# Kernel optimization log

Measured on AMD Instinct MI355X. Metric: run time of the kernel, lower is better.

The kernel has to match this reference:

```python
import jax, jax.numpy as jnp
import numpy as np
from jax import lax

V_VOX, T_PTS, D, H, W = 12000, 35, 10, 200, 176
EPS = 1e-5


def _bn(x, g, b, axes, shape):
    m = x.mean(axes, keepdims=True)
    v = x.var(axes, keepdims=True)  # biased var, matches torch BN training stats
    return g.reshape(shape) * (x - m) * lax.rsqrt(v + EPS) + b.reshape(shape)


def _conv3d(x, w, b):
    y = lax.conv_general_dilated(x, w, (1, 1, 1), 'SAME',
                                 dimension_numbers=('NCDHW', 'OIDHW', 'NCDHW'))
    return y + b[None, :, None, None, None]


def _conv2d(x, w, b):
    y = lax.conv_general_dilated(x, w, (1, 1), 'SAME',
                                 dimension_numbers=('NCHW', 'OIHW', 'NCHW'))
    return y + b[None, :, None, None]


def setup_inputs() -> dict:
    key = jax.random.key(0)
    ks = jax.random.split(key, 12)
    voxels = jax.random.normal(ks[0], (1, V_VOX, T_PTS, 4), jnp.float32)
    # unique voxel coordinates (the torch loop overwrites on duplicates; unique avoids ambiguity)
    rng = np.random.default_rng(0)
    flat = rng.choice(D * H * W, size=V_VOX, replace=False)
    z = flat // (H * W); rem = flat % (H * W)
    coords = jnp.asarray(np.stack([z, rem // W, rem % W], axis=1), dtype=jnp.int32)
    s = 0.05
    p = dict(
        w_lin=jax.random.normal(ks[1], (32, 4), jnp.float32) * s,
        b_lin=jnp.zeros((32,), jnp.float32),
        g_bn0=jnp.ones((32,), jnp.float32), be_bn0=jnp.zeros((32,), jnp.float32),
        w_c3a=jax.random.normal(ks[2], (64, 32, 3, 3, 3), jnp.float32) * s,
        b_c3a=jnp.zeros((64,), jnp.float32),
        g_bn1=jnp.ones((64,), jnp.float32), be_bn1=jnp.zeros((64,), jnp.float32),
        w_c3b=jax.random.normal(ks[3], (64, 64, 3, 3, 3), jnp.float32) * s,
        b_c3b=jnp.zeros((64,), jnp.float32),
        g_bn2=jnp.ones((64,), jnp.float32), be_bn2=jnp.zeros((64,), jnp.float32),
        w_r1=jax.random.normal(ks[4], (128, 64, 3, 3), jnp.float32) * s,
        b_r1=jnp.zeros((128,), jnp.float32),
        w_r2=jax.random.normal(ks[5], (8, 128, 1, 1), jnp.float32) * s,
        b_r2=jnp.zeros((8,), jnp.float32),
    )
    return dict(voxels=voxels, coords=coords, **p)


def reference(voxels, coords, w_lin, b_lin, g_bn0, be_bn0,
              w_c3a, b_c3a, g_bn1, be_bn1, w_c3b, b_c3b, g_bn2, be_bn2,
              w_r1, b_r1, w_r2, b_r2):
    B, V, T, C = voxels.shape
    # SimpleVFE: linear -> BN1d (batch stats) -> relu -> max over points
    h = voxels.reshape(B * V * T, C) @ w_lin.T + b_lin          # [BVT,32]
    h = jax.nn.relu(_bn(h, g_bn0, be_bn0, 0, (1, 32)))
    feats = h.reshape(B, V, T, 32).max(axis=2)                  # [B,V,32]
    # fused scatter into dense volume (replaces per-voxel python loop)
    volume = jnp.zeros((B, 32, D, H, W), voxels.dtype)
    volume = volume.at[0, :, coords[:, 0], coords[:, 1], coords[:, 2]].set(feats[0])
    # 3D backbone
    x = jax.nn.relu(_bn(_conv3d(volume, w_c3a, b_c3a), g_bn1, be_bn1, (0, 2, 3, 4), (1, 64, 1, 1, 1)))
    x = jax.nn.relu(_bn(_conv3d(x, w_c3b, b_c3b), g_bn2, be_bn2, (0, 2, 3, 4), (1, 64, 1, 1, 1)))
    x = x.mean(axis=2)                                          # collapse depth -> [B,64,H,W]
    # RPN head
    out = _conv2d(jax.nn.relu(_conv2d(x, w_r1, b_r1)), w_r2, b_r2)  # [B,8,H,W]
    box = jnp.concatenate([out[:, 0:3], jnp.exp(out[:, 3:6]),
                           jnp.tanh(out[:, 6:7]), jax.nn.sigmoid(out[:, 7:8])], axis=1)
    return box
```

## Files before the change

kernel.cpp:

```cpp
#include <hip/hip_runtime.h>
#include <math.h>

#define V_VOX 12000
#define T_PTS 35
#define DD 10
#define HH 200
#define WW 176
#define EPSV 1e-5f

#define DP 12
#define HP 202
#define WP 178
#define PPLN (HP * WP)
#define PVOX (DP * PPLN)
#define NPIX (DD * HH * WW)
#define HWPIX (HH * WW)

typedef _Float16 half_t;
typedef _Float16 f16x8 __attribute__((ext_vector_type(8)));
typedef float f32x16 __attribute__((ext_vector_type(16)));

#define WPA_OFF 0
#define WPB_OFF 110592
#define WPR1_OFF 331776
#define STATS_OFF 479232
#define FEATS_OFF 483328
#define VOLP_OFF 2019328
#define X1P_OFF 29633536
#define Y_OFF 84861952
#define PLANE_OFF 129917952
#define R1OUT_OFF 134520320

#define S_BN0S 0
#define S_BN0Q 32
#define S_BN1S 64
#define S_BN1Q 128
#define S_BN2S 192
#define S_BN2Q 256
#define C0A 320
#define C0B 352
#define C1A 384
#define C1B 448
#define C2A 512
#define C2B 576

__device__ __forceinline__ void gload16(const half_t* g, half_t* l) {
    __builtin_amdgcn_global_load_lds(
        (const __attribute__((address_space(1))) void*)g,
        (__attribute__((address_space(3))) void*)l, 16, 0, 0);
}

__global__ void k_pack(const float* __restrict__ w, half_t* __restrict__ wp,
                       int IC, int NT, int OC) {
    int id = blockIdx.x * 256 + threadIdx.x;
    int OCT = OC >> 5, KH = IC >> 5;
    int total = NT * KH * 2 * OCT * 512;
    if (id >= total) return;
    int j = id & 7;
    int lane = (id >> 3) & 63;
    int rest = id >> 9;
    int ot = rest % OCT; rest /= OCT;
    int khf = rest & 1; rest >>= 1;
    int kh = rest % KH;
    int tap = rest / KH;
    int oc = ot * 32 + (lane & 31);
    int ic = kh * 32 + khf * 16 + (lane >> 5) * 8 + j;
    wp[id] = (half_t)w[(oc * IC + ic) * NT + tap];
}

__global__ void k_vfe_stats(const float4* __restrict__ vox, const float* __restrict__ w_lin,
                            const float* __restrict__ b_lin, float* __restrict__ S) {
    int tid = blockIdx.x * 256 + threadIdx.x;
    int c = threadIdx.x & 31;
    float4 w = ((const float4*)w_lin)[c];
    float bl = b_lin[c];
    float s = 0.f, q = 0.f;
    const int np = V_VOX * T_PTS;
    int stride = gridDim.x * 8;
    for (int p = tid >> 5; p < np; p += stride) {
        float4 v = vox[p];
        float d = v.x * w.x + v.y * w.y + v.z * w.z + v.w * w.w + bl;
        s += d;
        q += d * d;
    }
    s += __shfl_xor(s, 32);
    q += __shfl_xor(q, 32);
    if ((threadIdx.x & 63) < 32) {
        atomicAdd(&S[S_BN0S + c], s);
        atomicAdd(&S[S_BN0Q + c], q);
    }
}

__global__ void k_bn_final(const float* __restrict__ ss, const float* __restrict__ sq,
                           const float* __restrict__ g, const float* __restrict__ be,
                           float* __restrict__ ca, float* __restrict__ cb, int C, float invN) {
    int c = threadIdx.x;
    if (c >= C) return;
    float m = ss[c] * invN;
    float v = sq[c] * invN - m * m;
    float a = g[c] * rsqrtf(v + EPSV);
    ca[c] = a;
    cb[c] = be[c] - m * a;
}

__global__ void k_vfe_max(const float4* __restrict__ vox, const float* __restrict__ w_lin,
                          const float* __restrict__ b_lin, const float* __restrict__ ca,
                          const float* __restrict__ cb, float* __restrict__ feats) {
    int id = blockIdx.x * 256 + threadIdx.x;
    if (id >= V_VOX * 32) return;
    int c = id & 31;
    int v = id >> 5;
    float4 w = ((const float4*)w_lin)[c];
    float bl = b_lin[c], A = ca[c], B = cb[c];
    float m = 0.f;
    for (int t = 0; t < T_PTS; t++) {
        float4 p = vox[v * T_PTS + t];
        float d = p.x * w.x + p.y * w.y + p.z * w.z + p.w * w.w + bl;
        m = fmaxf(m, A * d + B);
    }
    feats[id] = m;
}

__global__ void k_scatter(const float* __restrict__ feats, const int* __restrict__ coords,
                          half_t* __restrict__ volp) {
    int id = blockIdx.x * 256 + threadIdx.x;
    if (id >= V_VOX * 32) return;
    int c = id & 31;
    int v = id >> 5;
    int z = coords[v * 3 + 0];
    int y = coords[v * 3 + 1];
    int x = coords[v * 3 + 2];
    volp[(((z + 1) * HP + (y + 1)) * WP + (x + 1)) * 32 + c] = (half_t)feats[id];
}

template <int KH, int DZ, int OCALL, bool RELU, bool STATS>
__global__ __launch_bounds__(512, 4) void k_conv(const half_t* __restrict__ in,
                                                 size_t khstride,
                                                 const half_t* __restrict__ wp,
                                                 const float* __restrict__ bias,
                                                 half_t* __restrict__ out,
                                                 float* __restrict__ ssum,
                                                 float* __restrict__ ssq) {
    constexpr int OCT = OCALL / 32;
    constexpr int NS = DZ * KH;
    __shared__ __align__(16) half_t tA[1296 * 8];
    __shared__ __align__(16) half_t tB[36 * 512];

    const int tid = threadIdx.x;
    const int lane = tid & 63;
    const int wv = tid >> 6;
    const int yg = wv >> 1;
    const int og = wv & 1;
    const int x0 = blockIdx.x * 16;
    const int y0b = blockIdx.y * 16;
    const int bz = blockIdx.z;
    const int z0 = (DZ == 3) ? bz : 0;
    const int ocb = (DZ == 3) ? 0 : bz * 2;
    const bool valid = (y0b + yg * 4 < HH);
    const int xl = lane & 15;
    const int yrl = (lane >> 4) & 1;
    const int kg = (lane >> 5) & 1;

    int gofsA[3]; bool okA[3];
#pragma unroll
    for (int r = 0; r < 3; ++r) {
        int c = tid + r * 512;
        okA[r] = (c < 1296);
        int cc = okA[r] ? c : 0;
        int p0 = ((cc >> 2) ^ (cc >> 4)) & 1;
        int p = ((cc >> 3) << 1) | p0;
        int q = (cc & 3) ^ (p & 3);
        int row = p / 18, px = p - row * 18;
        int grow = y0b + row;
        if (grow > HP - 1) grow = HP - 1;
        gofsA[r] = (grow * WP + x0 + px) * 32 + q * 8;
    }

    f32x16 acc[2];
#pragma unroll
    for (int m = 0; m < 2; ++m) acc[m] = (f32x16)(0.f);

    auto STAGE = [&](int s) {
        const int dz = s / KH, kh = s % KH;
        const half_t* sl = in + (size_t)kh * khstride
                           + (size_t)(z0 + dz) * (DZ == 3 ? (size_t)PPLN * 32 : 0);
#pragma unroll
        for (int r = 0; r < 3; ++r)
            if (okA[r]) gload16(sl + gofsA[r], &tA[(size_t)(tid + r * 512) * 8]);
#pragma unroll
        for (int r = 0; r < 5; ++r) {
            int c = tid + r * 512;
            if (c < 2304) {
                int u = c >> 6;
                int tl = u >> 2, khf = (u >> 1) & 1, ot = u & 1;
                const half_t* g = wp + ((((size_t)(dz * 9 + tl) * KH + kh) * 2 + khf) * OCT
                                        + ocb + ot) * 512 + lane * 8;
                gload16(g, &tB[(size_t)u * 512 + lane * 8]);
            }
        }
    };

#pragma unroll 1
    for (int s = 0; s < NS; ++s) {
        STAGE(s);
        asm volatile("s_waitcnt vmcnt(0)" ::: "memory");
        __syncthreads();

        if (valid) {
#pragma unroll
            for (int khalf = 0; khalf < 2; ++khalf) {
#pragma unroll
                for (int dx = 0; dx < 3; ++dx) {
#pragma unroll
                    for (int dy = 0; dy < 3; ++dy) {
                        int u = ((dy * 3 + dx) * 2 + khalf) * 2 + og;
                        f16x8 Bf = *(const f16x8*)&tB[u * 512 + lane * 8];
#pragma unroll
                        for (int m = 0; m < 2; ++m) {
                            int p = (yg * 4 + dy + 2 * m + yrl) * 18 + dx + xl;
                            int ph = ((p << 6) | ((khalf * 2 + kg) << 4)) ^ ((p & 7) << 4);
                            f16x8 Af = *(const f16x8*)((const char*)tA + ph);
                            acc[m] = __builtin_amdgcn_mfma_f32_32x32x16_f16(
                                Af, Bf, acc[m], 0, 0, 0);
                        }
                    }
                }
            }
        }
        __syncthreads();
    }

    if (!valid) return;
    float sreg = 0.f, qreg = 0.f;
    int oc = (ocb + og) * 32 + (lane & 31);
    float bv = bias[oc];
#pragma unroll
    for (int m = 0; m < 2; ++m) {
#pragma unroll
        for (int reg = 0; reg < 16; ++reg) {
            int rp = (reg & 3) + 8 * (reg >> 2) + 4 * kg;
            int xx = x0 + (rp & 15);
            int yy = y0b + yg * 4 + 2 * m + (rp >> 4);
            float v = acc[m][reg] + bv;
            if (STATS) { sreg += v; qreg += v * v; }
            float w = RELU ? fmaxf(v, 0.f) : v;
            out[((size_t)(z0 * HH + yy) * WW + xx) * OCALL + oc] = (half_t)w;
        }
    }
    if (STATS) {
        sreg += __shfl_xor(sreg, 32);
        qreg += __shfl_xor(qreg, 32);
        if (lane < 32) {
            atomicAdd(&ssum[oc], sreg);
            atomicAdd(&ssq[oc], qreg);
        }
    }
}

__global__ void k_activate(const half_t* __restrict__ y1, const float* __restrict__ ca,
                           const float* __restrict__ cb, half_t* __restrict__ xp) {
    int id = blockIdx.x * 256 + threadIdx.x;
    if (id >= PVOX * 8) return;
    int c0 = (id & 7) * 8;
    int pix = id >> 3;
    int zp = pix / PPLN;
    int rem = pix - zp * PPLN;
    int yp = rem / WP;
    int xq = rem - yp * WP;
    f16x8 o;
    if (zp >= 1 && zp <= DD && yp >= 1 && yp <= HH && xq >= 1 && xq <= WW) {
        size_t p = ((size_t)((zp - 1) * HH + (yp - 1)) * WW + (xq - 1));
        f16x8 v = *(const f16x8*)(y1 + p * 64 + c0);
#pragma unroll
        for (int j = 0; j < 8; j++)
            o[j] = (half_t)fmaxf(ca[c0 + j] * (float)v[j] + cb[c0 + j], 0.f);
    } else {
#pragma unroll
        for (int j = 0; j < 8; j++) o[j] = (half_t)0.f;
    }
    int khp = c0 >> 5;
    *(f16x8*)(xp + (size_t)khp * PVOX * 32 + (size_t)pix * 32 + (c0 & 31)) = o;
}

__global__ void k_depthmean(const half_t* __restrict__ y2, const float* __restrict__ ca,
                            const float* __restrict__ cb, half_t* __restrict__ plane) {
    int id = blockIdx.x * 256 + threadIdx.x;
    int c = id & 63;
    int pix = id >> 6;
    int yp = pix / WP;
    int xq = pix - yp * WP;
    float val = 0.f;
    if (yp >= 1 && yp <= HH && xq >= 1 && xq <= WW) {
        float A = ca[c], B = cb[c], s = 0.f;
        const half_t* base = y2 + ((size_t)(yp - 1) * WW + (xq - 1)) * 64 + c;
#pragma unroll
        for (int z = 0; z < DD; z++)
            s += fmaxf(A * (float)base[(size_t)z * HWPIX * 64] + B, 0.f);
        val = s * 0.1f;
    }
    int khp = c >> 5;
    plane[(size_t)khp * PPLN * 32 + (size_t)pix * 32 + (c & 31)] = (half_t)val;
}

__global__ void k_r2(const half_t* __restrict__ r1o, const float* __restrict__ w,
                     const float* __restrict__ bias, float* __restrict__ outp) {
    __shared__ float wsm[1024];
    for (int i = threadIdx.x; i < 1024; i += 256) wsm[i] = w[i];
    __syncthreads();
    int p = blockIdx.x * 256 + threadIdx.x;
    if (p >= HWPIX) return;
    float acc[8];
#pragma unroll
    for (int o = 0; o < 8; o++) acc[o] = bias[o];
    const half_t* rb = r1o + (size_t)p * 128;
#pragma unroll 4
    for (int icb = 0; icb < 128; icb += 8) {
        f16x8 v = *(const f16x8*)(rb + icb);
#pragma unroll
        for (int j = 0; j < 8; j++) {
            float vv = (float)v[j];
#pragma unroll
            for (int o = 0; o < 8; o++) acc[o] += vv * wsm[o * 128 + icb + j];
        }
    }
    outp[0 * HWPIX + p] = acc[0];
    outp[1 * HWPIX + p] = acc[1];
    outp[2 * HWPIX + p] = acc[2];
    outp[3 * HWPIX + p] = expf(acc[3]);
    outp[4 * HWPIX + p] = expf(acc[4]);
    outp[5 * HWPIX + p] = expf(acc[5]);
    outp[6 * HWPIX + p] = tanhf(acc[6]);
    outp[7 * HWPIX + p] = 1.f / (1.f + expf(-acc[7]));
}

extern "C" void kernel_launch(void* const* d_in, const int* in_sizes, int n_in,
                              void* d_out, int out_size, void* d_ws, size_t ws_size,
                              hipStream_t stream) {
    const float4* voxels = (const float4*)d_in[0];
    const int* coords = (const int*)d_in[1];
    const float* w_lin = (const float*)d_in[2];
    const float* b_lin = (const float*)d_in[3];
    const float* g_bn0 = (const float*)d_in[4];
    const float* be_bn0 = (const float*)d_in[5];
    const float* w_c3a = (const float*)d_in[6];
    const float* b_c3a = (const float*)d_in[7];
    const float* g_bn1 = (const float*)d_in[8];
    const float* be_bn1 = (const float*)d_in[9];
    const float* w_c3b = (const float*)d_in[10];
    const float* b_c3b = (const float*)d_in[11];
    const float* g_bn2 = (const float*)d_in[12];
    const float* be_bn2 = (const float*)d_in[13];
    const float* w_r1 = (const float*)d_in[14];
    const float* b_r1 = (const float*)d_in[15];
    const float* w_r2 = (const float*)d_in[16];
    const float* b_r2 = (const float*)d_in[17];

    char* ws = (char*)d_ws;
    half_t* wpA = (half_t*)(ws + WPA_OFF);
    half_t* wpB = (half_t*)(ws + WPB_OFF);
    half_t* wpR1 = (half_t*)(ws + WPR1_OFF);
    float* S = (float*)(ws + STATS_OFF);
    float* feats = (float*)(ws + FEATS_OFF);
    half_t* volp = (half_t*)(ws + VOLP_OFF);
    half_t* x1p = (half_t*)(ws + X1P_OFF);
    half_t* Y = (half_t*)(ws + Y_OFF);
    half_t* plane = (half_t*)(ws + PLANE_OFF);
    half_t* r1out = (half_t*)(ws + R1OUT_OFF);
    float* outp = (float*)d_out;

    hipMemsetAsync(S, 0, 320 * sizeof(float), stream);
    hipMemsetAsync(volp, 0, (size_t)PVOX * 32 * sizeof(half_t), stream);

    k_pack<<<216, 256, 0, stream>>>(w_c3a, wpA, 32, 27, 64);
    k_pack<<<432, 256, 0, stream>>>(w_c3b, wpB, 64, 27, 64);
    k_pack<<<288, 256, 0, stream>>>(w_r1, wpR1, 64, 9, 128);

    k_vfe_stats<<<512, 256, 0, stream>>>(voxels, w_lin, b_lin, S);
    k_bn_final<<<1, 64, 0, stream>>>(S + S_BN0S, S + S_BN0Q, g_bn0, be_bn0,
                                     S + C0A, S + C0B, 32, 1.f / 420000.f);
    k_vfe_max<<<1500, 256, 0, stream>>>(voxels, w_lin, b_lin, S + C0A, S + C0B, feats);
    k_scatter<<<1500, 256, 0, stream>>>(feats, coords, volp);

    k_conv<1, 3, 64, false, true><<<dim3(11, 13, 10), 512, 0, stream>>>(
        volp, 0, wpA, b_c3a, Y, S + S_BN1S, S + S_BN1Q);
    k_bn_final<<<1, 64, 0, stream>>>(S + S_BN1S, S + S_BN1Q, g_bn1, be_bn1,
                                     S + C1A, S + C1B, 64, 1.f / 352000.f);
    k_activate<<<13484, 256, 0, stream>>>(Y, S + C1A, S + C1B, x1p);

    k_conv<2, 3, 64, false, true><<<dim3(11, 13, 10), 512, 0, stream>>>(
        x1p, (size_t)PVOX * 32, wpB, b_c3b, Y, S + S_BN2S, S + S_BN2Q);
    k_bn_final<<<1, 64, 0, stream>>>(S + S_BN2S, S + S_BN2Q, g_bn2, be_bn2,
                                     S + C2A, S + C2B, 64, 1.f / 352000.f);

    k_depthmean<<<8989, 256, 0, stream>>>(Y, S + C2A, S + C2B, plane);

    k_conv<2, 1, 128, true, false><<<dim3(11, 13, 2), 512, 0, stream>>>(
        plane, (size_t)PPLN * 32, wpR1, b_r1, r1out, nullptr, nullptr);
    k_r2<<<138, 256, 0, stream>>>(r1out, w_r2, b_r2, outp);
}
```

Measured before the change: 468.4 us.

## Give each conv wave both output-channel tiles, halving block size to 256 threads

The conv kernel now uses 4 waves per block instead of 8. Each wave computes a 2x2 grid of 32x32 MFMA tiles covering both output-channel groups, where before each wave owned one group. Each A fragment read from shared memory is now reused across two B fragments, which cuts LDS reads per MFMA. The cost is twice the accumulator registers per wave, fewer waves for latency hiding, and more global-to-LDS staging work per thread.

Result: no change. 472.0 us (+0.8%).

```diff
diff --git a/kernel.cpp b/kernel.cpp
--- a/kernel.cpp
+++ b/kernel.cpp
@@ -133,24 +133,22 @@
     volp[(((z + 1) * HP + (y + 1)) * WP + (x + 1)) * 32 + c] = (half_t)feats[id];
 }
 
-template <int KH, int DZ, int OCALL, bool RELU, bool STATS>
-__global__ __launch_bounds__(512, 4) void k_conv(const half_t* __restrict__ in,
+template <int KH, int DZ, int OCT, bool RELU, bool STATS>
+__global__ __launch_bounds__(256, 2) void k_conv(const half_t* __restrict__ in,
                                                  size_t khstride,
                                                  const half_t* __restrict__ wp,
                                                  const float* __restrict__ bias,
                                                  half_t* __restrict__ out,
                                                  float* __restrict__ ssum,
                                                  float* __restrict__ ssq) {
-    constexpr int OCT = OCALL / 32;
+    constexpr int OCALL = OCT * 32;
     constexpr int NS = DZ * KH;
     __shared__ __align__(16) half_t tA[1296 * 8];
     __shared__ __align__(16) half_t tB[36 * 512];
 
     const int tid = threadIdx.x;
     const int lane = tid & 63;
-    const int wv = tid >> 6;
-    const int yg = wv >> 1;
-    const int og = wv & 1;
+    const int yg = tid >> 6;
     const int x0 = blockIdx.x * 16;
     const int y0b = blockIdx.y * 16;
     const int bz = blockIdx.z;
@@ -161,10 +159,10 @@
     const int yrl = (lane >> 4) & 1;
     const int kg = (lane >> 5) & 1;
 
-    int gofsA[3]; bool okA[3];
-#pragma unroll
-    for (int r = 0; r < 3; ++r) {
-        int c = tid + r * 512;
+    int gofsA[6]; bool okA[6];
+#pragma unroll
+    for (int r = 0; r < 6; ++r) {
+        int c = tid + r * 256;
         okA[r] = (c < 1296);
         int cc = okA[r] ? c : 0;
         int p0 = ((cc >> 2) ^ (cc >> 4)) & 1;
@@ -176,27 +174,28 @@
         gofsA[r] = (grow * WP + x0 + px) * 32 + q * 8;
     }
 
-    f32x16 acc[2];
-#pragma unroll
-    for (int m = 0; m < 2; ++m) acc[m] = (f32x16)(0.f);
+    f32x16 acc[2][2];
+#pragma unroll
+    for (int m = 0; m < 2; ++m)
+#pragma unroll
+        for (int n = 0; n < 2; ++n) acc[m][n] = (f32x16)(0.f);
 
     auto STAGE = [&](int s) {
         const int dz = s / KH, kh = s % KH;
         const half_t* sl = in + (size_t)kh * khstride
                            + (size_t)(z0 + dz) * (DZ == 3 ? (size_t)PPLN * 32 : 0);
 #pragma unroll
-        for (int r = 0; r < 3; ++r)
-            if (okA[r]) gload16(sl + gofsA[r], &tA[(size_t)(tid + r * 512) * 8]);
-#pragma unroll
-        for (int r = 0; r < 5; ++r) {
-            int c = tid + r * 512;
-            if (c < 2304) {
-                int u = c >> 6;
-                int tl = u >> 2, khf = (u >> 1) & 1, ot = u & 1;
-                const half_t* g = wp + ((((size_t)(dz * 9 + tl) * KH + kh) * 2 + khf) * OCT
-                                        + ocb + ot) * 512 + lane * 8;
-                gload16(g, &tB[(size_t)u * 512 + lane * 8]);
-            }
+        for (int r = 0; r < 6; ++r)
+            if (okA[r]) gload16(sl + gofsA[r], &tA[(size_t)(tid + r * 256) * 8]);
+#pragma unroll
+        for (int r = 0; r < 9; ++r) {
+            int c = tid + r * 256;
+            int u = c >> 6;
+            int l64 = c & 63;
+            int tl = u >> 2, khf = (u >> 1) & 1, ot = u & 1;
+            const half_t* g = wp + ((((size_t)(dz * 9 + tl) * KH + kh) * 2 + khf) * OCT
+                                    + ocb + ot) * 512 + l64 * 8;
+            gload16(g, &tB[(size_t)u * 512 + l64 * 8]);
         }
     };
 
@@ -213,16 +212,24 @@
                 for (int dx = 0; dx < 3; ++dx) {
 #pragma unroll
                     for (int dy = 0; dy < 3; ++dy) {
-                        int u = ((dy * 3 + dx) * 2 + khalf) * 2 + og;
-                        f16x8 Bf = *(const f16x8*)&tB[u * 512 + lane * 8];
+                        int u = ((dy * 3 + dx) * 2 + khalf) * 2;
+                        f16x8 Bf[2];
+#pragma unroll
+                        for (int n = 0; n < 2; ++n)
+                            Bf[n] = *(const f16x8*)&tB[(u + n) * 512 + lane * 8];
+                        f16x8 Af[2];
 #pragma unroll
                         for (int m = 0; m < 2; ++m) {
                             int p = (yg * 4 + dy + 2 * m + yrl) * 18 + dx + xl;
                             int ph = ((p << 6) | ((khalf * 2 + kg) << 4)) ^ ((p & 7) << 4);
-                            f16x8 Af = *(const f16x8*)((const char*)tA + ph);
-                            acc[m] = __builtin_amdgcn_mfma_f32_32x32x16_f16(
-                                Af, Bf, acc[m], 0, 0, 0);
+                            Af[m] = *(const f16x8*)((const char*)tA + ph);
                         }
+#pragma unroll
+                        for (int m = 0; m < 2; ++m)
+#pragma unroll
+                            for (int n = 0; n < 2; ++n)
+                                acc[m][n] = __builtin_amdgcn_mfma_f32_32x32x16_f16(
+                                    Af[m], Bf[n], acc[m][n], 0, 0, 0);
                     }
                 }
             }
@@ -231,28 +238,36 @@
     }
 
     if (!valid) return;
-    float sreg = 0.f, qreg = 0.f;
-    int oc = (ocb + og) * 32 + (lane & 31);
-    float bv = bias[oc];
-#pragma unroll
-    for (int m = 0; m < 2; ++m) {
-#pragma unroll
-        for (int reg = 0; reg < 16; ++reg) {
-            int rp = (reg & 3) + 8 * (reg >> 2) + 4 * kg;
-            int xx = x0 + (rp & 15);
-            int yy = y0b + yg * 4 + 2 * m + (rp >> 4);
-            float v = acc[m][reg] + bv;
-            if (STATS) { sreg += v; qreg += v * v; }
-            float w = RELU ? fmaxf(v, 0.f) : v;
-            out[((size_t)(z0 * HH + yy) * WW + xx) * OCALL + oc] = (half_t)w;
+    float sreg[2] = {0.f, 0.f}, qreg[2] = {0.f, 0.f};
+#pragma unroll
+    for (int n = 0; n < 2; ++n) {
+        int oc = (ocb + n) * 32 + (lane & 31);
+        float bv = bias[oc];
+#pragma unroll
+        for (int m = 0; m < 2; ++m) {
+#pragma unroll
+            for (int reg = 0; reg < 16; ++reg) {
+                int rp = (reg & 3) + 8 * (reg >> 2) + 4 * kg;
+                int xx = x0 + (rp & 15);
+                int yy = y0b + yg * 4 + 2 * m + (rp >> 4);
+                float v = acc[m][n][reg] + bv;
+                if (STATS) { sreg[n] += v; qreg[n] += v * v; }
+                float w = RELU ? fmaxf(v, 0.f) : v;
+                out[((size_t)(z0 * HH + yy) * WW + xx) * OCALL + oc] = (half_t)w;
+            }
         }
     }
     if (STATS) {
-        sreg += __shfl_xor(sreg, 32);
-        qreg += __shfl_xor(qreg, 32);
-        if (lane < 32) {
-            atomicAdd(&ssum[oc], sreg);
-            atomicAdd(&ssq[oc], qreg);
+#pragma unroll
+        for (int n = 0; n < 2; ++n) {
+            float s = sreg[n], q = qreg[n];
+            s += __shfl_xor(s, 32);
+            q += __shfl_xor(q, 32);
+            if (lane < 32) {
+                int oc = (ocb + n) * 32 + lane;
+                atomicAdd(&ssum[oc], s);
+                atomicAdd(&ssq[oc], q);
+            }
         }
     }
 }
@@ -381,20 +396,20 @@
     k_vfe_max<<<1500, 256, 0, stream>>>(voxels, w_lin, b_lin, S + C0A, S + C0B, feats);
     k_scatter<<<1500, 256, 0, stream>>>(feats, coords, volp);
 
-    k_conv<1, 3, 64, false, true><<<dim3(11, 13, 10), 512, 0, stream>>>(
+    k_conv<1, 3, 2, false, true><<<dim3(11, 13, 10), 256, 0, stream>>>(
         volp, 0, wpA, b_c3a, Y, S + S_BN1S, S + S_BN1Q);
     k_bn_final<<<1, 64, 0, stream>>>(S + S_BN1S, S + S_BN1Q, g_bn1, be_bn1,
                                      S + C1A, S + C1B, 64, 1.f / 352000.f);
     k_activate<<<13484, 256, 0, stream>>>(Y, S + C1A, S + C1B, x1p);
 
-    k_conv<2, 3, 64, false, true><<<dim3(11, 13, 10), 512, 0, stream>>>(
+    k_conv<2, 3, 2, false, true><<<dim3(11, 13, 10), 256, 0, stream>>>(
         x1p, (size_t)PVOX * 32, wpB, b_c3b, Y, S + S_BN2S, S + S_BN2Q);
     k_bn_final<<<1, 64, 0, stream>>>(S + S_BN2S, S + S_BN2Q, g_bn2, be_bn2,
                                      S + C2A, S + C2B, 64, 1.f / 352000.f);
 
     k_depthmean<<<8989, 256, 0, stream>>>(Y, S + C2A, S + C2B, plane);
 
-    k_conv<2, 1, 128, true, false><<<dim3(11, 13, 2), 512, 0, stream>>>(
+    k_conv<2, 1, 4, true, false><<<dim3(11, 13, 2), 256, 0, stream>>>(
         plane, (size_t)PPLN * 32, wpR1, b_r1, r1out, nullptr, nullptr);
     k_r2<<<138, 256, 0, stream>>>(r1out, w_r2, b_r2, outp);
 }
```
